# Kernel optimization log

Hardware: AMD Instinct MI355X
Metric: run time of the kernel (lower is better)

Reference implementation:

```python
import jax, jax.numpy as jnp
import numpy as np


def gru_layer(x, h0, Wih, Whh, bih, bhh):
    """Run a single-direction PyTorch-style GRU over x: [B,T,D] -> ([B,T,H], [B,H]).
    Gate order matches torch (r, z, n)."""
    xg = jnp.einsum('btd,gd->btg', x, Wih) + bih  # precompute input gates [B,T,3H]

    def step(h, gi):
        gh = h @ Whh.T + bhh
        ir, iz, inn = jnp.split(gi, 3, axis=-1)
        hr, hz, hn = jnp.split(gh, 3, axis=-1)
        r = jax.nn.sigmoid(ir + hr)
        z = jax.nn.sigmoid(iz + hz)
        n = jnp.tanh(inn + r * hn)
        h_new = (1.0 - z) * n + z * h
        return h_new, h_new

    hT, ys = jax.lax.scan(step, h0, jnp.swapaxes(xg, 0, 1))
    return jnp.swapaxes(ys, 0, 1), hT


def setup_inputs() -> dict:
    key = jax.random.key(0)
    ks = jax.random.split(key, 13)
    B, T, D, H = 64, 100, 75, 1024
    s = 0.02
    rn = lambda k, shp: (jax.random.normal(k, shp, jnp.float32) * s)
    return {
        'input_tensor': jax.random.normal(ks[0], (B, T, D), jnp.float32),
        'seq_len': jax.random.randint(ks[1], (B,), 1, T + 1, jnp.int32),
        'enc_Wih0': rn(ks[2], (2, 3 * H, D)),
        'enc_Whh0': rn(ks[3], (2, 3 * H, H)),
        'enc_b0': rn(ks[4], (2, 2, 3 * H)),
        'enc_Wih': rn(ks[5], (2, 2, 3 * H, 2 * H)),
        'enc_Whh': rn(ks[6], (2, 2, 3 * H, H)),
        'enc_b': rn(ks[7], (2, 2, 2, 3 * H)),
        'dec_Wih': rn(ks[8], (6 * H, D)),
        'dec_Whh': rn(ks[9], (6 * H, 2 * H)),
        'dec_b': rn(ks[10], (2, 6 * H)),
        'out_W': rn(ks[11], (D, 2 * H)),
        'out_b': rn(ks[12], (D,)),
    }


def reference(input_tensor, seq_len, enc_Wih0, enc_Whh0, enc_b0,
              enc_Wih, enc_Whh, enc_b, dec_Wih, dec_Whh, dec_b,
              out_W, out_b):
    B, T, D = input_tensor.shape
    H = enc_Whh0.shape[-1]
    h0 = jnp.zeros((B, H), input_tensor.dtype)

    # Encoder: the original feeds the bidirectional GRU one timestep at a time,
    # so BOTH direction parameter sets run left-to-right (degenerate bidir).
    yf, _ = gru_layer(input_tensor, h0, enc_Wih0[0], enc_Whh0[0], enc_b0[0, 0], enc_b0[0, 1])
    yb, _ = gru_layer(input_tensor, h0, enc_Wih0[1], enc_Whh0[1], enc_b0[1, 0], enc_b0[1, 1])
    y = jnp.concatenate([yf, yb], axis=-1)  # [B,T,2H]
    for l in range(enc_Wih.shape[0]):  # layers 1..num_layers-1
        yf, _ = gru_layer(y, h0, enc_Wih[l, 0], enc_Whh[l, 0], enc_b[l, 0, 0], enc_b[l, 0, 1])
        yb, _ = gru_layer(y, h0, enc_Wih[l, 1], enc_Whh[l, 1], enc_b[l, 1, 0], enc_b[l, 1, 1])
        y = jnp.concatenate([yf, yb], axis=-1)

    sl = jnp.clip(seq_len, 1, T)
    enc_hidden = y[jnp.arange(B), sl - 1][None]  # (1, B, 2H): last valid step per sample

    # Decoder: 1-layer GRU (hidden 2H) over a zeros input sequence, init = enc_hidden
    de_in = jnp.zeros_like(input_tensor)
    ys, _ = gru_layer(de_in, enc_hidden[0], dec_Wih, dec_Whh, dec_b[0], dec_b[1])
    dec_out = ys @ out_W.T + out_b  # [B,T,D]
    return (enc_hidden, dec_out)
```

## Files before the change

### kernel.cpp

```cpp
#include <hip/hip_runtime.h>
#include <math.h>

typedef unsigned short u16;
typedef unsigned long long u64;
typedef __attribute__((ext_vector_type(8))) short s16x8;
typedef __attribute__((ext_vector_type(4))) short s16x4;
typedef __attribute__((ext_vector_type(4))) float f4v;

__device__ __forceinline__ float bf2f(short u) {
    union { unsigned int i; float f; } v;
    v.i = ((unsigned int)(u16)u) << 16;
    return v.f;
}
__device__ __forceinline__ u16 f2bf(float f) {
    union { float f; unsigned int i; } v; v.f = f;
    unsigned int x = v.i;
    return (u16)((x + 0x7FFFu + ((x >> 16) & 1u)) >> 16);
}

__device__ __forceinline__ u64 coh_load_u64(const u16* p) {
    return __hip_atomic_load((const u64*)p, __ATOMIC_RELAXED, __HIP_MEMORY_SCOPE_AGENT);
}
__device__ __forceinline__ void coh_store_u64(u16* p, u64 v) {
    __hip_atomic_store((u64*)p, v, __ATOMIC_RELAXED, __HIP_MEMORY_SCOPE_AGENT);
}
__device__ __forceinline__ unsigned flag_load(const unsigned* p) {
    return __hip_atomic_load(p, __ATOMIC_RELAXED, __HIP_MEMORY_SCOPE_AGENT);
}
__device__ __forceinline__ void flag_store(unsigned* p, unsigned v) {
    __hip_atomic_store(p, v, __ATOMIC_RELAXED, __HIP_MEMORY_SCOPE_AGENT);
}

__device__ __forceinline__ void flag_barrier(unsigned* slot, int nblk, unsigned tgt) {
    __syncthreads();
    if (threadIdx.x == 0)
        flag_store(&slot[blockIdx.x], tgt);
    if (blockIdx.x == 0 && (int)threadIdx.x < 64) {
        int spins = 0;
        for (;;) {
            int ok = 1;
            for (int i = (int)threadIdx.x; i < nblk; i += 64)
                ok &= (flag_load(&slot[i]) >= tgt);
            if (__all(ok)) break;
            __builtin_amdgcn_s_sleep(2);
            if (++spins > (1 << 20)) break;
        }
        if (threadIdx.x == 0)
            flag_store(&slot[192], tgt);
    }
    if (threadIdx.x == 0) {
        int spins2 = 0;
        while (flag_load(&slot[192]) < tgt) {
            __builtin_amdgcn_s_sleep(1);
            if (++spins2 > (1 << 20)) break;
        }
    }
    __syncthreads();
    asm volatile("" ::: "memory");
}

__global__ void zero_bar(unsigned* p, int n) {
    int i = blockIdx.x * blockDim.x + threadIdx.x;
    if (i < n) p[i] = 0;
}

__global__ __launch_bounds__(256)
void cvt_bf16v(const float* __restrict__ src, u16* __restrict__ dst, int n4) {
    int i = blockIdx.x * 256 + threadIdx.x;
    int stride = gridDim.x * 256;
    for (; i < n4; i += stride) {
        f4v v = ((const f4v*)src)[i];
        s16x4 o;
#pragma unroll
        for (int j = 0; j < 4; ++j) o[j] = (short)f2bf(v[j]);
        ((s16x4*)dst)[i] = o;
    }
}

__global__ __launch_bounds__(256)
void cvt_pack(const float* __restrict__ src, u16* __restrict__ dst,
              int JT, int KB, int K)
{
    int fid = blockIdx.x * 4 + (threadIdx.x >> 6);
    int lane = threadIdx.x & 63;
    int nf = 3 * JT * KB;
    if (fid >= nf) return;
    int g = fid / (JT * KB);
    int rem = fid - g * JT * KB;
    int jt = rem / KB;
    int kb = rem - jt * KB;
    int j = jt * 16 + (lane & 15);
    int k = kb * 32 + (lane >> 4) * 8;
    const float* s = src + ((size_t)g * JT * 16 + j) * K + k;
    f4v a = *(const f4v*)s;
    f4v b = *(const f4v*)(s + 4);
    s16x8 o;
#pragma unroll
    for (int i = 0; i < 4; ++i) { o[i] = (short)f2bf(a[i]); o[4 + i] = (short)f2bf(b[i]); }
    *(s16x8*)(dst + (size_t)fid * 512 + lane * 8) = o;
}

__global__ __launch_bounds__(256)
void xg0_kernel(const float* __restrict__ x,
                const float* __restrict__ W,
                const float* __restrict__ bih,
                u16* __restrict__ xg)
{
    const int bt0 = blockIdx.x * 16;
    __shared__ float xl[16][76];
    for (int idx = threadIdx.x; idx < 16 * 75; idx += 256) {
        int r = idx / 75, k = idx % 75;
        xl[r][k] = x[(size_t)(bt0 + r) * 75 + k];
    }
    __syncthreads();
    for (int i = 0; i < 12; ++i) {
        int g = threadIdx.x + i * 256;
        const float* wr = W + (size_t)g * 75;
        float bv = bih[g];
        float acc[16];
#pragma unroll
        for (int r = 0; r < 16; ++r) acc[r] = bv;
        for (int k = 0; k < 75; ++k) {
            float w = wr[k];
#pragma unroll
            for (int r = 0; r < 16; ++r) acc[r] += xl[r][k] * w;
        }
#pragma unroll
        for (int r = 0; r < 16; ++r)
            xg[(size_t)(bt0 + r) * 3072 + g] = f2bf(acc[r]);
    }
}

__global__ __launch_bounds__(256)
void xg_gemm2(const u16* __restrict__ A, const float* __restrict__ Bm,
              const float* __restrict__ bias, u16* __restrict__ C, int K)
{
    __shared__ u16 Alds[128 * 40];
    __shared__ u16 Blds[64 * 40];
    const int bid = blockIdx.x;
    const int xcd = bid & 7;
    const int r = bid >> 3;
    const int n_t = xcd * 6 + r % 6;
    const int m_t = r / 6;
    const int m0 = m_t * 128;
    const int n0 = n_t * 64;
    const int tid = threadIdx.x;
    const int wv = tid >> 6;
    const int lane = tid & 63;
    const int kq = (lane >> 4) * 8;
    const int col = lane & 15;
    f4v acc[2][4];
#pragma unroll
    for (int am = 0; am < 2; ++am)
#pragma unroll
        for (int nt = 0; nt < 4; ++nt) acc[am][nt] = (f4v){0.f, 0.f, 0.f, 0.f};

    for (int k0 = 0; k0 < K; k0 += 32) {
#pragma unroll
        for (int i = 0; i < 2; ++i) {
            int c = tid * 2 + i;
            int row = c >> 2, kk = (c & 3) * 8;
            *(s16x8*)&Alds[row * 40 + kk] =
                *(const s16x8*)(A + (size_t)(m0 + row) * K + k0 + kk);
        }
        {
            int row = tid >> 2, kk = (tid & 3) * 8;
            f4v b0v = *(const f4v*)(Bm + (size_t)(n0 + row) * K + k0 + kk);
            f4v b1v = *(const f4v*)(Bm + (size_t)(n0 + row) * K + k0 + kk + 4);
            s16x8 bb;
#pragma unroll
            for (int i = 0; i < 4; ++i) { bb[i] = (short)f2bf(b0v[i]); bb[4 + i] = (short)f2bf(b1v[i]); }
            *(s16x8*)&Blds[row * 40 + kk] = bb;
        }
        __syncthreads();
        s16x8 a0 = *(const s16x8*)&Alds[(wv * 32 + (lane & 15)) * 40 + kq];
        s16x8 a1 = *(const s16x8*)&Alds[(wv * 32 + 16 + (lane & 15)) * 40 + kq];
#pragma unroll
        for (int nt = 0; nt < 4; ++nt) {
            s16x8 b = *(const s16x8*)&Blds[(nt * 16 + (lane & 15)) * 40 + kq];
            acc[0][nt] = __builtin_amdgcn_mfma_f32_16x16x32_bf16(a0, b, acc[0][nt], 0, 0, 0);
            acc[1][nt] = __builtin_amdgcn_mfma_f32_16x16x32_bf16(a1, b, acc[1][nt], 0, 0, 0);
        }
        __syncthreads();
    }
    const int rq = (lane >> 4) * 4;
#pragma unroll
    for (int am = 0; am < 2; ++am)
#pragma unroll
    for (int nt = 0; nt < 4; ++nt) {
        int n = n0 + nt * 16 + col;
        float bv = bias[n];
#pragma unroll
        for (int rg = 0; rg < 4; ++rg) {
            int m = m0 + wv * 32 + am * 16 + rq + rg;
            C[(size_t)m * 3072 + n] = f2bf(acc[am][nt][rg] + bv);
        }
    }
}

__global__ __launch_bounds__(256)
void enc_persist(const u16* __restrict__ Wp,
                 const float* __restrict__ bias,
                 const u16* __restrict__ xg,
                 u16* __restrict__ hbf,
                 u16* __restrict__ y,
                 int dir, unsigned* __restrict__ bar)
{
    __shared__ u16 Al[16 * 1024];
    __shared__ u16 OutE[16 * 64];
    const int tid = threadIdx.x;
    const int lane = tid & 63;
    const int wv = tid >> 6;
    const int xcd = blockIdx.x & 7;
    const int jg = xcd * 2 + ((blockIdx.x >> 3) & 1);
    const int bq = blockIdx.x >> 4;
    const int b0 = bq * 16;
    unsigned* flags = bar + bq * 64;
    const int jc = jg * 64 + wv * 16 + (lane & 15);
    const int jt = jg * 4 + wv;
    const int kq = (lane >> 4) * 8;
    const int arow = lane & 15;
    const int axor = (arow & 7) << 3;
    const float bhr = bias[3072 + jc];
    const float bhz = bias[4096 + jc];
    const float bhn = bias[5120 + jc];
    const u16* pW[3];
    pW[0] = Wp + ((size_t)(0 * 64 + jt) * 32) * 512 + lane * 8;
    pW[1] = Wp + ((size_t)(1 * 64 + jt) * 32) * 512 + lane * 8;
    pW[2] = Wp + ((size_t)(2 * 64 + jt) * 32) * 512 + lane * 8;
    const int brow = b0 + (lane >> 4) * 4;
    const int srow = tid >> 4;
    const int sci  = tid & 15;
    f4v hold = {0.f, 0.f, 0.f, 0.f};

    for (int t = 0; t < 100; ++t) {
        f4v aR = {0.f, 0.f, 0.f, 0.f}, aZ = aR, aN = aR;
        if (t > 0) {
            const u16* hb = hbf + (size_t)(t & 1) * 65536 + (size_t)b0 * 1024;
            {
                u64 v = coh_load_u64(hb + (size_t)srow * 1024 + jg * 64 + sci * 4);
                int c = srow * 128 + jg * 8 + (sci >> 1);
                int di = (c * 8) ^ ((srow & 7) << 3);
                *(u64*)&Al[di + (sci & 1) * 4] = v;
            }
            unsigned pending = 0xFFFFu & ~(1u << jg);
            int spins = 0;
            while (pending) {
                unsigned fv = flag_load(&flags[lane & 15]);
                unsigned ready = (unsigned)__ballot(fv >= (unsigned)t) & 0xFFFFu;
                unsigned newly = ready & pending;
                if (newly) {
                    u64 v[16];
#pragma unroll
                    for (int p = 0; p < 16; ++p)
                        if (newly & (1u << p))
                            v[p] = coh_load_u64(hb + (size_t)srow * 1024 + p * 64 + sci * 4);
#pragma unroll
                    for (int p = 0; p < 16; ++p)
                        if (newly & (1u << p)) {
                            int c = srow * 128 + p * 8 + (sci >> 1);
                            int di = (c * 8) ^ ((srow & 7) << 3);
                            *(u64*)&Al[di + (sci & 1) * 4] = v[p];
                        }
                    pending &= ~newly;
                }
                if (pending) {
                    __builtin_amdgcn_s_sleep(1);
                    if (++spins > (1 << 20)) break;
                }
            }
            __syncthreads();
            const int abase = arow * 1024 + kq;
            s16x8 W[2][3][4];
#pragma unroll
            for (int g = 0; g < 3; ++g)
#pragma unroll
                for (int q = 0; q < 4; ++q)
                    W[0][g][q] = *(const s16x8*)(pW[g] + (size_t)q * 512);
#pragma unroll
            for (int bt = 0; bt < 8; ++bt) {
                if (bt < 7) {
#pragma unroll
                    for (int g = 0; g < 3; ++g)
#pragma unroll
                        for (int q = 0; q < 4; ++q)
                            W[(bt + 1) & 1][g][q] =
                                *(const s16x8*)(pW[g] + (size_t)((bt + 1) * 4 + q) * 512);
                }
#pragma unroll
                for (int q = 0; q < 4; ++q) {
                    s16x8 av = *(const s16x8*)&Al[(abase + (bt * 4 + q) * 32) ^ axor];
                    aR = __builtin_amdgcn_mfma_f32_16x16x32_bf16(av, W[bt & 1][0][q], aR, 0, 0, 0);
                    aZ = __builtin_amdgcn_mfma_f32_16x16x32_bf16(av, W[bt & 1][1][q], aZ, 0, 0, 0);
                    aN = __builtin_amdgcn_mfma_f32_16x16x32_bf16(av, W[bt & 1][2][q], aN, 0, 0, 0);
                }
            }
        }
#pragma unroll
        for (int r = 0; r < 4; ++r) {
            int b = brow + r;
            const u16* xr = xg + ((size_t)b * 100 + t) * 3072;
            float pr = bf2f((short)xr[jc]) + aR[r] + bhr;
            float pz = bf2f((short)xr[1024 + jc]) + aZ[r] + bhz;
            float pn = bf2f((short)xr[2048 + jc]);
            float rg = 1.f / (1.f + expf(-pr));
            float zg = 1.f / (1.f + expf(-pz));
            float ng = tanhf(pn + rg * (aN[r] + bhn));
            float hnew = (1.f - zg) * ng + zg * hold[r];
            hold[r] = hnew;
            OutE[((lane >> 4) * 4 + r) * 64 + wv * 16 + (lane & 15)] = f2bf(hnew);
        }
        __syncthreads();
        if (tid < 128) {
            int bl = tid >> 3, jl = (tid & 7) * 8;
            s16x8 v = *(const s16x8*)&OutE[bl * 64 + jl];
            const u64* pv = (const u64*)&v;
            u16* hw = hbf + (size_t)((t + 1) & 1) * 65536
                    + (size_t)(b0 + bl) * 1024 + jg * 64 + jl;
            coh_store_u64(hw, pv[0]);
            coh_store_u64(hw + 4, pv[1]);
            *(s16x8*)(y + ((size_t)(b0 + bl) * 100 + t) * 2048
                        + (size_t)dir * 1024 + jg * 64 + jl) = v;
        }
        if (t < 99) {
            __syncthreads();
            if (tid == 0) flag_store(&flags[jg], (unsigned)(t + 1));
        }
    }
}

__global__ __launch_bounds__(256)
void dec_persist(const u16* __restrict__ Wp,
                 const float* __restrict__ db,
                 const float* __restrict__ h32,
                 u16* __restrict__ hbf,
                 u16* __restrict__ ys,
                 unsigned* __restrict__ bar)
{
    __shared__ u16 Al[16 * 2048];
    __shared__ u16 OutD[16 * 64];
    const int tid = threadIdx.x;
    const int lane = tid & 63;
    const int wv = tid >> 6;
    const int xcd = blockIdx.x & 7;
    const int idx = blockIdx.x >> 3;
    const int jg = xcd * 4 + (idx & 3);
    const int b0 = (idx >> 2) * 16;
    const int jc = jg * 64 + wv * 16 + (lane & 15);
    const int jt = jg * 4 + wv;
    const int kq = (lane >> 4) * 8;
    const int arow = lane & 15;
    const int axor = (arow & 7) << 3;
    const float gir = db[jc]        + db[6144 + jc];
    const float giz = db[2048 + jc] + db[8192 + jc];
    const float gin = db[4096 + jc];
    const float bhn = db[10240 + jc];
    const u16* pR = Wp + ((size_t)(0 * 128 + jt) * 64) * 512 + lane * 8;
    const u16* pZ = Wp + ((size_t)(1 * 128 + jt) * 64) * 512 + lane * 8;
    const u16* pN = Wp + ((size_t)(2 * 128 + jt) * 64) * 512 + lane * 8;
    f4v hold;
#pragma unroll
    for (int r = 0; r < 4; ++r)
        hold[r] = h32[(size_t)(b0 + (lane >> 4) * 4 + r) * 2048 + jc];

    for (int t = 0; t < 100; ++t) {
        const u16* hb = hbf + (size_t)(t & 1) * 131072 + (size_t)b0 * 2048;
#pragma unroll
        for (int h = 0; h < 2; ++h) {
            u64 tmp[16];
#pragma unroll
            for (int g = 0; g < 8; ++g) {
                int c = tid + (h * 8 + g) * 256;
                const u16* gp = hb + (size_t)(c >> 8) * 2048 + (c & 255) * 8;
                tmp[2 * g]     = coh_load_u64(gp);
                tmp[2 * g + 1] = coh_load_u64(gp + 4);
            }
#pragma unroll
            for (int g = 0; g < 8; ++g) {
                int c = tid + (h * 8 + g) * 256;
                int di = (c * 8) ^ (((c >> 8) & 7) << 3);
                *(u64*)&Al[di]     = tmp[2 * g];
                *(u64*)&Al[di + 4] = tmp[2 * g + 1];
            }
        }
        __syncthreads();
        f4v aR = {0.f, 0.f, 0.f, 0.f}, aZ = aR, aN = aR;
        const int abase = arow * 2048 + kq;
        s16x8 cR = *(const s16x8*)(pR);
        s16x8 cZ = *(const s16x8*)(pZ);
        s16x8 cN = *(const s16x8*)(pN);
        for (int kb = 0; kb < 64; ++kb) {
            int kn = (kb + 1 < 64) ? kb + 1 : kb;
            s16x8 nR = *(const s16x8*)(pR + (size_t)kn * 512);
            s16x8 nZ = *(const s16x8*)(pZ + (size_t)kn * 512);
            s16x8 nN = *(const s16x8*)(pN + (size_t)kn * 512);
            s16x8 av = *(const s16x8*)&Al[(abase + kb * 32) ^ axor];
            aR = __builtin_amdgcn_mfma_f32_16x16x32_bf16(av, cR, aR, 0, 0, 0);
            aZ = __builtin_amdgcn_mfma_f32_16x16x32_bf16(av, cZ, aZ, 0, 0, 0);
            aN = __builtin_amdgcn_mfma_f32_16x16x32_bf16(av, cN, aN, 0, 0, 0);
            cR = nR; cZ = nZ; cN = nN;
        }
        __syncthreads();
#pragma unroll
        for (int r = 0; r < 4; ++r) {
            float pr = gir + aR[r];
            float pz = giz + aZ[r];
            float rg = 1.f / (1.f + expf(-pr));
            float zg = 1.f / (1.f + expf(-pz));
            float ng = tanhf(gin + rg * (aN[r] + bhn));
            float hnew = (1.f - zg) * ng + zg * hold[r];
            hold[r] = hnew;
            OutD[((lane >> 4) * 4 + r) * 64 + wv * 16 + (lane & 15)] = f2bf(hnew);
        }
        __syncthreads();
        if (tid < 128) {
            int bl = tid >> 3, jl = (tid & 7) * 8;
            s16x8 v = *(const s16x8*)&OutD[bl * 64 + jl];
            const u64* pv = (const u64*)&v;
            u16* hw = hbf + (size_t)((t + 1) & 1) * 131072
                    + (size_t)(b0 + bl) * 2048 + jg * 64 + jl;
            coh_store_u64(hw, pv[0]);
            coh_store_u64(hw + 4, pv[1]);
            *(s16x8*)(ys + ((size_t)(b0 + bl) * 100 + t) * 2048 + jg * 64 + jl) = v;
        }
        if (t < 99) flag_barrier(bar, 128, (unsigned)(t + 1));
    }
}

__global__ __launch_bounds__(256)
void gather_kernel(const int* __restrict__ seq_len, const u16* __restrict__ y,
                   float* __restrict__ out_enc, float* __restrict__ h32d,
                   u16* __restrict__ hbfd)
{
    int idx = blockIdx.x * 256 + threadIdx.x;
    int b = idx >> 11, j = idx & 2047;
    int s = seq_len[b];
    s = s < 1 ? 1 : (s > 100 ? 100 : s);
    u16 v = y[((size_t)b * 100 + (s - 1)) * 2048 + j];
    float f = bf2f((short)v);
    out_enc[idx] = f;
    h32d[idx] = f;
    hbfd[idx] = v;
}

__global__ __launch_bounds__(256)
void proj_kernel(const u16* __restrict__ ys, const float* __restrict__ oW,
                 const float* __restrict__ oB, float* __restrict__ dec_out)
{
    const int r0 = blockIdx.x * 8;
    __shared__ float yl[8][2048];
    __shared__ float psum[3][8][76];
    for (int idx = threadIdx.x; idx < 2048; idx += 256) {
        int rr = idx >> 8, cc = idx & 255;
        s16x8 v = ((const s16x8*)(ys + (size_t)(r0 + rr) * 2048))[cc];
#pragma unroll
        for (int i = 0; i < 8; ++i) yl[rr][cc * 8 + i] = bf2f(v[i]);
    }
    __syncthreads();
    if (threadIdx.x < 225) {
        int d = threadIdx.x % 75, seg = threadIdx.x / 75;
        int ks = seg * 683, ke = ks + 683 < 2048 ? ks + 683 : 2048;
        const float* wr = oW + (size_t)d * 2048;
        float acc[8] = {0.f, 0.f, 0.f, 0.f, 0.f, 0.f, 0.f, 0.f};
        for (int k = ks; k < ke; ++k) {
            float w = wr[k];
#pragma unroll
            for (int r = 0; r < 8; ++r) acc[r] += yl[r][k] * w;
        }
#pragma unroll
        for (int r = 0; r < 8; ++r) psum[seg][r][d] = acc[r];
    }
    __syncthreads();
    for (int idx = threadIdx.x; idx < 600; idx += 256) {
        int r = idx / 75, d = idx % 75;
        dec_out[(size_t)(r0 + r) * 75 + d] =
            psum[0][r][d] + psum[1][r][d] + psum[2][r][d] + oB[d];
    }
}

__device__ __forceinline__ void gemv3_f32(const float* __restrict__ w0,
                                          const float* __restrict__ w1,
                                          const float* __restrict__ w2,
                                          const f4v* __restrict__ hv,
                                          int n4, float& a0, float& a1, float& a2)
{
    for (int k = 0; k < n4; ++k) {
        f4v h4 = hv[k];
        f4v x0 = *(const f4v*)(w0 + k * 4);
        f4v x1 = *(const f4v*)(w1 + k * 4);
        f4v x2 = *(const f4v*)(w2 + k * 4);
        a0 += h4[0]*x0[0] + h4[1]*x0[1] + h4[2]*x0[2] + h4[3]*x0[3];
        a1 += h4[0]*x1[0] + h4[1]*x1[1] + h4[2]*x1[2] + h4[3]*x1[3];
        a2 += h4[0]*x2[0] + h4[1]*x2[1] + h4[2]*x2[2] + h4[3]*x2[3];
    }
}
__device__ __forceinline__ float dot_w32_v32(const float* __restrict__ w,
                                             const float* __restrict__ v, int n)
{
    float a = 0.f;
    for (int k = 0; k < n; ++k) a += w[k] * v[k];
    return a;
}
__device__ __forceinline__ float dot_w32_vbf(const float* __restrict__ w,
                                             const u16* __restrict__ v, int n8)
{
    float a = 0.f;
    for (int k8 = 0; k8 < n8; ++k8) {
        s16x8 v8 = *(const s16x8*)(v + k8 * 8);
        f4v w0 = *(const f4v*)(w + k8 * 8);
        f4v w1 = *(const f4v*)(w + k8 * 8 + 4);
        a += w0[0]*bf2f(v8[0]) + w0[1]*bf2f(v8[1]) + w0[2]*bf2f(v8[2]) + w0[3]*bf2f(v8[3])
           + w1[0]*bf2f(v8[4]) + w1[1]*bf2f(v8[5]) + w1[2]*bf2f(v8[6]) + w1[3]*bf2f(v8[7]);
    }
    return a;
}

__global__ __launch_bounds__(512)
void enc_scan_fused(int t,
                    const float* __restrict__ h_in, float* __restrict__ h_out,
                    const float* __restrict__ Whh, size_t whh_stride,
                    const float* __restrict__ Wih, size_t wih_stride, int Kin,
                    const float* __restrict__ xf, const u16* __restrict__ xb,
                    const float* __restrict__ bias, int bias_stride,
                    u16* __restrict__ y)
{
    const int dir = blockIdx.z;
    const int jt = blockIdx.x;
    const int b0 = blockIdx.y * 16;
    __shared__ float hlds[16][1024];
    const float* hin = h_in + (size_t)dir * 65536 + (size_t)b0 * 1024;
    if (t == 0) {
        f4v z = {0.f, 0.f, 0.f, 0.f};
        for (int idx = threadIdx.x; idx < 4096; idx += 512) ((f4v*)hlds)[idx] = z;
    } else {
        for (int idx = threadIdx.x; idx < 4096; idx += 512)
            ((f4v*)hlds)[idx] = ((const f4v*)hin)[idx];
    }
    __syncthreads();
    const int jl = threadIdx.x & 31;
    const int j  = jt * 32 + jl;
    const int bp = threadIdx.x >> 5;
    const float* wd = Whh + (size_t)dir * whh_stride;
    float a0 = 0.f, a1 = 0.f, a2 = 0.f;
    gemv3_f32(wd + (size_t)j * 1024, wd + (size_t)(1024 + j) * 1024,
              wd + (size_t)(2048 + j) * 1024, (const f4v*)&hlds[bp][0], 256, a0, a1, a2);
    const float* bd = bias + dir * bias_stride;
    const float* wi = Wih + (size_t)dir * wih_stride;
    const int gb = b0 + bp;
    float gi[3];
#pragma unroll
    for (int g = 0; g < 3; ++g) {
        const float* wr = wi + (size_t)(g * 1024 + j) * Kin;
        float s;
        if (xf) s = dot_w32_v32(wr, xf + ((size_t)gb * 100 + t) * Kin, Kin);
        else    s = dot_w32_vbf(wr, xb + ((size_t)gb * 100 + t) * Kin, Kin >> 3);
        gi[g] = bd[g * 1024 + j] + s;
    }
    const float* bhh = bd + 3072;
    float pr = gi[0] + a0 + bhh[j];
    float pz = gi[1] + a1 + bhh[1024 + j];
    float rg = 1.f / (1.f + expf(-pr));
    float zg = 1.f / (1.f + expf(-pz));
    float ng = tanhf(gi[2] + rg * (a2 + bhh[2048 + j]));
    float hold = hlds[bp][j];
    float hnew = (1.f - zg) * ng + zg * hold;
    h_out[(size_t)dir * 65536 + (size_t)gb * 1024 + j] = hnew;
    y[((size_t)gb * 100 + t) * 2048 + (size_t)dir * 1024 + j] = f2bf(hnew);
}

__global__ __launch_bounds__(512)
void dec_scan_step(int t, const float* __restrict__ h_in, float* __restrict__ h_out,
                   const float* __restrict__ Whh, const float* __restrict__ db,
                   u16* __restrict__ ys)
{
    const int jt = blockIdx.x;
    const int b0 = blockIdx.y * 16;
    __shared__ float hlds[16][1024];
    const int jl = threadIdx.x & 31;
    const int j  = jt * 32 + jl;
    const int bp = threadIdx.x >> 5;
    float a0 = 0.f, a1 = 0.f, a2 = 0.f;
    float hold = 0.f;
    for (int kc = 0; kc < 2; ++kc) {
        for (int idx = threadIdx.x; idx < 4096; idx += 512) {
            int rr = idx >> 8, cc = idx & 255;
            ((f4v*)hlds)[idx] = *(const f4v*)(h_in + (size_t)(b0 + rr) * 2048 + kc * 1024 + cc * 4);
        }
        __syncthreads();
        if ((j >> 10) == kc) hold = hlds[bp][j & 1023];
        const float* wb = Whh + kc * 1024;
        gemv3_f32(wb + (size_t)j * 2048, wb + (size_t)(2048 + j) * 2048,
                  wb + (size_t)(4096 + j) * 2048, (const f4v*)&hlds[bp][0], 256, a0, a1, a2);
        __syncthreads();
    }
    const int gb = b0 + bp;
    float pr = db[j] + a0 + db[6144 + j];
    float pz = db[2048 + j] + a1 + db[6144 + 2048 + j];
    float rg = 1.f / (1.f + expf(-pr));
    float zg = 1.f / (1.f + expf(-pz));
    float ng = tanhf(db[4096 + j] + rg * (a2 + db[6144 + 4096 + j]));
    float hnew = (1.f - zg) * ng + zg * hold;
    h_out[(size_t)gb * 2048 + j] = hnew;
    ys[((size_t)gb * 100 + t) * 2048 + j] = f2bf(hnew);
}

extern "C" void kernel_launch(void* const* d_in, const int* in_sizes, int n_in,
                              void* d_out, int out_size, void* d_ws, size_t ws_size,
                              hipStream_t stream)
{
    const float* x    = (const float*)d_in[0];
    const int*   sl   = (const int*)d_in[1];
    const float* Wih0 = (const float*)d_in[2];
    const float* Whh0 = (const float*)d_in[3];
    const float* b0   = (const float*)d_in[4];
    const float* Wih  = (const float*)d_in[5];
    const float* Whh  = (const float*)d_in[6];
    const float* bE   = (const float*)d_in[7];
    const float* dWhh = (const float*)d_in[9];
    const float* dB   = (const float*)d_in[10];
    const float* oW   = (const float*)d_in[11];
    const float* oB   = (const float*)d_in[12];
    float* out_enc = (float*)d_out;
    float* dec_out = (float*)d_out + 131072;

    char* ws = (char*)d_ws;
    const size_t XG_OFF   = 0;
    const size_t YA_OFF   = 39321600;
    const size_t YB_OFF   = 65536000;
    const size_t WC_OFF   = 91750400;
    const size_t HBFE_OFF = 98566144;
    const size_t H32D_OFF = 98828288;
    const size_t HBFD_OFF = 99876864;
    const size_t BAR_OFF  = 100401152;
    const size_t NEED     = 100408320;

    dim3 blk256(256), blk512(512);

    if (ws_size >= NEED) {
        u16*   xg   = (u16*)(ws + XG_OFF);
        u16*   y_a  = (u16*)(ws + YA_OFF);
        u16*   y_b  = (u16*)(ws + YB_OFF);
        u16*   Wc   = (u16*)(ws + WC_OFF);
        u16*   hbfE = (u16*)(ws + HBFE_OFF);
        float* h32D = (float*)(ws + H32D_OFF);
        u16*   hbfD = (u16*)(ws + HBFD_OFF);
        unsigned* bar = (unsigned*)(ws + BAR_OFF);

        zero_bar<<<dim3(7), blk256, 0, stream>>>(bar, 1792);

        int slot = 0;
        for (int l = 0; l < 3; ++l) {
            const u16* y_in = (l == 0) ? (const u16*)0 : ((l == 1) ? y_a : y_b);
            u16* y_out      = (l == 2) ? y_a : ((l == 0) ? y_a : y_b);
            for (int d = 0; d < 2; ++d) {
                const float* Wsrc = (l == 0) ? (Whh0 + (size_t)d * 3145728)
                                             : (Whh + ((size_t)(l - 1) * 2 + d) * 3145728);
                const float* bias = (l == 0) ? (b0 + (size_t)d * 6144)
                                             : (bE + (size_t)(l - 1) * 12288 + (size_t)d * 6144);
                cvt_pack<<<dim3(1536), blk256, 0, stream>>>(Wsrc, Wc, 64, 32, 1024);
                if (l == 0)
                    xg0_kernel<<<dim3(400), blk256, 0, stream>>>(
                        x, Wih0 + (size_t)d * 230400, b0 + (size_t)d * 6144, xg);
                else
                    xg_gemm2<<<dim3(2400), blk256, 0, stream>>>(
                        y_in, Wih + ((size_t)(l - 1) * 2 + d) * 6291456, bias, xg, 2048);
                enc_persist<<<dim3(64), blk256, 0, stream>>>(
                    Wc, bias, xg, hbfE, y_out, d, bar + (size_t)slot * 256);
                ++slot;
            }
        }
        gather_kernel<<<dim3(512), blk256, 0, stream>>>(sl, y_a, out_enc, h32D, hbfD);
        u16* decW = (u16*)(ws + XG_OFF);
        cvt_pack<<<dim3(6144), blk256, 0, stream>>>(dWhh, decW, 128, 64, 2048);
        dec_persist<<<dim3(128), blk256, 0, stream>>>(decW, dB, h32D, hbfD, y_b,
                                                      bar + (size_t)6 * 256);
        proj_kernel<<<dim3(800), blk256, 0, stream>>>(y_b, oW, oB, dec_out);
    } else {
        const size_t Y_B = 26214400;
        u16*   y_a  = (u16*)ws;
        u16*   y_b  = (u16*)(ws + Y_B);
        float* hE   = (float*)(ws + 2 * Y_B);
        float* h32D = (float*)(ws + 2 * Y_B + 1048576);
        u16*   hbfD = (u16*)(ws + 2 * Y_B + 2097152);

        for (int t = 0; t < 100; ++t) {
            int pp = t & 1;
            enc_scan_fused<<<dim3(32, 4, 2), blk512, 0, stream>>>(
                t, hE + (size_t)pp * 131072, hE + (size_t)(pp ^ 1) * 131072,
                Whh0, (size_t)3145728, Wih0, (size_t)230400, 75, x, (const u16*)0,
                b0, 6144, y_a);
        }
        for (int l = 0; l < 2; ++l) {
            const u16* yin = (l == 0) ? y_a : y_b;
            u16* yout      = (l == 0) ? y_b : y_a;
            for (int t = 0; t < 100; ++t) {
                int pp = t & 1;
                enc_scan_fused<<<dim3(32, 4, 2), blk512, 0, stream>>>(
                    t, hE + (size_t)pp * 131072, hE + (size_t)(pp ^ 1) * 131072,
                    Whh + (size_t)l * 2 * 3145728, (size_t)3145728,
                    Wih + (size_t)l * 2 * 6291456, (size_t)6291456, 2048,
                    (const float*)0, yin, bE + (size_t)l * 12288, 6144, yout);
            }
        }
        gather_kernel<<<dim3(512), blk256, 0, stream>>>(sl, y_a, out_enc, h32D, hbfD);
        for (int t = 0; t < 100; ++t) {
            int pp = t & 1;
            dec_scan_step<<<dim3(64, 4), blk512, 0, stream>>>(
                t, h32D + (size_t)pp * 131072, h32D + (size_t)(pp ^ 1) * 131072, dWhh, dB, y_b);
        }
        proj_kernel<<<dim3(800), blk256, 0, stream>>>(y_b, oW, oB, dec_out);
    }
}
```

Baseline: 7.885 ms.

## Fuse input-gate GEMM into persistent encoder and run both directions concurrently

Removes the separate xg precompute kernels and computes the input-gate projection inside the persistent recurrent kernel each timestep, reading layer inputs straight from the previous layer's output. Both directions of a layer now run in one 128-block launch instead of two sequential 64-block launches, which halves the number of serialized recurrences. The cost is extra per-step work on the critical path: a 2048-deep GEMM per step streaming Wih from global memory, plus more LDS use (a 64KB Yl buffer). The Whh inner loop is also changed from register double-buffered tiles to simple one-ahead prefetching.

```diff
diff --git a/kernel.cpp b/kernel.cpp
--- a/kernel.cpp
+++ b/kernel.cpp
@@ -65,21 +65,8 @@
 }
 
 __global__ __launch_bounds__(256)
-void cvt_bf16v(const float* __restrict__ src, u16* __restrict__ dst, int n4) {
-    int i = blockIdx.x * 256 + threadIdx.x;
-    int stride = gridDim.x * 256;
-    for (; i < n4; i += stride) {
-        f4v v = ((const f4v*)src)[i];
-        s16x4 o;
-#pragma unroll
-        for (int j = 0; j < 4; ++j) o[j] = (short)f2bf(v[j]);
-        ((s16x4*)dst)[i] = o;
-    }
-}
-
-__global__ __launch_bounds__(256)
 void cvt_pack(const float* __restrict__ src, u16* __restrict__ dst,
-              int JT, int KB, int K)
+              int JT, int KB, int Kstride, int Ksrc)
 {
     int fid = blockIdx.x * 4 + (threadIdx.x >> 6);
     int lane = threadIdx.x & 63;
@@ -91,159 +78,110 @@
     int kb = rem - jt * KB;
     int j = jt * 16 + (lane & 15);
     int k = kb * 32 + (lane >> 4) * 8;
-    const float* s = src + ((size_t)g * JT * 16 + j) * K + k;
-    f4v a = *(const f4v*)s;
-    f4v b = *(const f4v*)(s + 4);
+    const float* s = src + ((size_t)g * JT * 16 + j) * Kstride + k;
     s16x8 o;
-#pragma unroll
-    for (int i = 0; i < 4; ++i) { o[i] = (short)f2bf(a[i]); o[4 + i] = (short)f2bf(b[i]); }
+    if (k + 8 <= Ksrc) {
+        f4v a = *(const f4v*)s;
+        f4v b = *(const f4v*)(s + 4);
+#pragma unroll
+        for (int i = 0; i < 4; ++i) { o[i] = (short)f2bf(a[i]); o[4 + i] = (short)f2bf(b[i]); }
+    } else {
+#pragma unroll
+        for (int e = 0; e < 8; ++e)
+            o[e] = (k + e < Ksrc) ? (short)f2bf(s[e]) : (short)0;
+    }
     *(s16x8*)(dst + (size_t)fid * 512 + lane * 8) = o;
 }
 
 __global__ __launch_bounds__(256)
-void xg0_kernel(const float* __restrict__ x,
-                const float* __restrict__ W,
-                const float* __restrict__ bih,
-                u16* __restrict__ xg)
-{
-    const int bt0 = blockIdx.x * 16;
-    __shared__ float xl[16][76];
-    for (int idx = threadIdx.x; idx < 16 * 75; idx += 256) {
-        int r = idx / 75, k = idx % 75;
-        xl[r][k] = x[(size_t)(bt0 + r) * 75 + k];
-    }
-    __syncthreads();
-    for (int i = 0; i < 12; ++i) {
-        int g = threadIdx.x + i * 256;
-        const float* wr = W + (size_t)g * 75;
-        float bv = bih[g];
-        float acc[16];
-#pragma unroll
-        for (int r = 0; r < 16; ++r) acc[r] = bv;
-        for (int k = 0; k < 75; ++k) {
-            float w = wr[k];
-#pragma unroll
-            for (int r = 0; r < 16; ++r) acc[r] += xl[r][k] * w;
-        }
-#pragma unroll
-        for (int r = 0; r < 16; ++r)
-            xg[(size_t)(bt0 + r) * 3072 + g] = f2bf(acc[r]);
-    }
-}
-
-__global__ __launch_bounds__(256)
-void xg_gemm2(const u16* __restrict__ A, const float* __restrict__ Bm,
-              const float* __restrict__ bias, u16* __restrict__ C, int K)
-{
-    __shared__ u16 Alds[128 * 40];
-    __shared__ u16 Blds[64 * 40];
-    const int bid = blockIdx.x;
-    const int xcd = bid & 7;
-    const int r = bid >> 3;
-    const int n_t = xcd * 6 + r % 6;
-    const int m_t = r / 6;
-    const int m0 = m_t * 128;
-    const int n0 = n_t * 64;
-    const int tid = threadIdx.x;
-    const int wv = tid >> 6;
-    const int lane = tid & 63;
-    const int kq = (lane >> 4) * 8;
-    const int col = lane & 15;
-    f4v acc[2][4];
-#pragma unroll
-    for (int am = 0; am < 2; ++am)
-#pragma unroll
-        for (int nt = 0; nt < 4; ++nt) acc[am][nt] = (f4v){0.f, 0.f, 0.f, 0.f};
-
-    for (int k0 = 0; k0 < K; k0 += 32) {
-#pragma unroll
-        for (int i = 0; i < 2; ++i) {
-            int c = tid * 2 + i;
-            int row = c >> 2, kk = (c & 3) * 8;
-            *(s16x8*)&Alds[row * 40 + kk] =
-                *(const s16x8*)(A + (size_t)(m0 + row) * K + k0 + kk);
-        }
-        {
-            int row = tid >> 2, kk = (tid & 3) * 8;
-            f4v b0v = *(const f4v*)(Bm + (size_t)(n0 + row) * K + k0 + kk);
-            f4v b1v = *(const f4v*)(Bm + (size_t)(n0 + row) * K + k0 + kk + 4);
-            s16x8 bb;
-#pragma unroll
-            for (int i = 0; i < 4; ++i) { bb[i] = (short)f2bf(b0v[i]); bb[4 + i] = (short)f2bf(b1v[i]); }
-            *(s16x8*)&Blds[row * 40 + kk] = bb;
-        }
-        __syncthreads();
-        s16x8 a0 = *(const s16x8*)&Alds[(wv * 32 + (lane & 15)) * 40 + kq];
-        s16x8 a1 = *(const s16x8*)&Alds[(wv * 32 + 16 + (lane & 15)) * 40 + kq];
-#pragma unroll
-        for (int nt = 0; nt < 4; ++nt) {
-            s16x8 b = *(const s16x8*)&Blds[(nt * 16 + (lane & 15)) * 40 + kq];
-            acc[0][nt] = __builtin_amdgcn_mfma_f32_16x16x32_bf16(a0, b, acc[0][nt], 0, 0, 0);
-            acc[1][nt] = __builtin_amdgcn_mfma_f32_16x16x32_bf16(a1, b, acc[1][nt], 0, 0, 0);
-        }
-        __syncthreads();
-    }
-    const int rq = (lane >> 4) * 4;
-#pragma unroll
-    for (int am = 0; am < 2; ++am)
-#pragma unroll
-    for (int nt = 0; nt < 4; ++nt) {
-        int n = n0 + nt * 16 + col;
-        float bv = bias[n];
-#pragma unroll
-        for (int rg = 0; rg < 4; ++rg) {
-            int m = m0 + wv * 32 + am * 16 + rq + rg;
-            C[(size_t)m * 3072 + n] = f2bf(acc[am][nt][rg] + bv);
-        }
-    }
-}
-
-__global__ __launch_bounds__(256)
-void enc_persist(const u16* __restrict__ Wp,
-                 const float* __restrict__ bias,
-                 const u16* __restrict__ xg,
-                 u16* __restrict__ hbf,
-                 u16* __restrict__ y,
-                 int dir, unsigned* __restrict__ bar)
-{
+void enc_fused(const u16* __restrict__ WihP, int wih_dfrags,
+               const u16* __restrict__ WhhP,
+               const float* __restrict__ bias,
+               const float* __restrict__ x,
+               const u16* __restrict__ yin,
+               u16* __restrict__ hbf,
+               u16* __restrict__ yout,
+               unsigned* __restrict__ bar)
+{
+    __shared__ u16 Yl[16 * 2048];
     __shared__ u16 Al[16 * 1024];
     __shared__ u16 OutE[16 * 64];
     const int tid = threadIdx.x;
     const int lane = tid & 63;
     const int wv = tid >> 6;
     const int xcd = blockIdx.x & 7;
-    const int jg = xcd * 2 + ((blockIdx.x >> 3) & 1);
-    const int bq = blockIdx.x >> 4;
+    const int dir = xcd >> 2;
+    const int idx = blockIdx.x >> 3;
+    const int jgd = (xcd & 3) * 4 + (idx & 3);
+    const int bq = idx >> 2;
     const int b0 = bq * 16;
-    unsigned* flags = bar + bq * 64;
-    const int jc = jg * 64 + wv * 16 + (lane & 15);
-    const int jt = jg * 4 + wv;
+    unsigned* flags = bar + (dir * 4 + bq) * 64;
+    const int jc = jgd * 64 + wv * 16 + (lane & 15);
+    const int jt = jgd * 4 + wv;
     const int kq = (lane >> 4) * 8;
     const int arow = lane & 15;
     const int axor = (arow & 7) << 3;
-    const float bhr = bias[3072 + jc];
-    const float bhz = bias[4096 + jc];
-    const float bhn = bias[5120 + jc];
+    const float* bd = bias + dir * 6144;
+    const float biasR = bd[jc] + bd[3072 + jc];
+    const float biasZ = bd[1024 + jc] + bd[4096 + jc];
+    const float bihN = bd[2048 + jc];
+    const float bhhN = bd[5120 + jc];
+    const u16* WihD = WihP + (size_t)dir * wih_dfrags * 512;
+    const u16* WhhD = WhhP + (size_t)dir * (3 * 64 * 32) * 512;
+    const int kbin = wih_dfrags / 192;
+    const u16* pXW[3];
     const u16* pW[3];
-    pW[0] = Wp + ((size_t)(0 * 64 + jt) * 32) * 512 + lane * 8;
-    pW[1] = Wp + ((size_t)(1 * 64 + jt) * 32) * 512 + lane * 8;
-    pW[2] = Wp + ((size_t)(2 * 64 + jt) * 32) * 512 + lane * 8;
+#pragma unroll
+    for (int g = 0; g < 3; ++g) {
+        pXW[g] = WihD + ((size_t)(g * 64 + jt) * kbin) * 512 + lane * 8;
+        pW[g]  = WhhD + ((size_t)(g * 64 + jt) * 32) * 512 + lane * 8;
+    }
     const int brow = b0 + (lane >> 4) * 4;
     const int srow = tid >> 4;
     const int sci  = tid & 15;
+    u16* hbfD = hbf + (size_t)dir * 131072;
     f4v hold = {0.f, 0.f, 0.f, 0.f};
 
+    if (x) {
+        for (int i = tid; i < 16 * 21; i += 256) {
+            int r = i / 21, k = 75 + i % 21;
+            Yl[r * 96 + k] = 0;
+        }
+    }
+
     for (int t = 0; t < 100; ++t) {
-        f4v aR = {0.f, 0.f, 0.f, 0.f}, aZ = aR, aN = aR;
+        if (x) {
+            for (int i = tid; i < 1200; i += 256) {
+                int r = i / 75, k = i % 75;
+                Yl[r * 96 + k] = f2bf(x[((size_t)(b0 + r) * 100 + t) * 75 + k]);
+            }
+        } else {
+#pragma unroll
+            for (int h2 = 0; h2 < 2; ++h2) {
+                s16x8 tmp[8];
+#pragma unroll
+                for (int g2 = 0; g2 < 8; ++g2) {
+                    int c = tid + (h2 * 8 + g2) * 256;
+                    int row = c >> 8, coli = c & 255;
+                    tmp[g2] = *(const s16x8*)(yin + ((size_t)(b0 + row) * 100 + t) * 2048 + coli * 8);
+                }
+#pragma unroll
+                for (int g2 = 0; g2 < 8; ++g2) {
+                    int c = tid + (h2 * 8 + g2) * 256;
+                    int di = (c * 8) ^ (((c >> 8) & 7) << 3);
+                    *(s16x8*)&Yl[di] = tmp[g2];
+                }
+            }
+        }
         if (t > 0) {
-            const u16* hb = hbf + (size_t)(t & 1) * 65536 + (size_t)b0 * 1024;
+            const u16* hb = hbfD + (size_t)(t & 1) * 65536 + (size_t)b0 * 1024;
             {
-                u64 v = coh_load_u64(hb + (size_t)srow * 1024 + jg * 64 + sci * 4);
-                int c = srow * 128 + jg * 8 + (sci >> 1);
+                u64 v = coh_load_u64(hb + (size_t)srow * 1024 + jgd * 64 + sci * 4);
+                int c = srow * 128 + jgd * 8 + (sci >> 1);
                 int di = (c * 8) ^ ((srow & 7) << 3);
                 *(u64*)&Al[di + (sci & 1) * 4] = v;
             }
-            unsigned pending = 0xFFFFu & ~(1u << jg);
+            unsigned pending = 0xFFFFu & ~(1u << jgd);
             int spins = 0;
             while (pending) {
                 unsigned fv = flag_load(&flags[lane & 15]);
@@ -269,43 +207,63 @@
                     if (++spins > (1 << 20)) break;
                 }
             }
-            __syncthreads();
-            const int abase = arow * 1024 + kq;
-            s16x8 W[2][3][4];
-#pragma unroll
-            for (int g = 0; g < 3; ++g)
-#pragma unroll
-                for (int q = 0; q < 4; ++q)
-                    W[0][g][q] = *(const s16x8*)(pW[g] + (size_t)q * 512);
-#pragma unroll
-            for (int bt = 0; bt < 8; ++bt) {
-                if (bt < 7) {
-#pragma unroll
-                    for (int g = 0; g < 3; ++g)
-#pragma unroll
-                        for (int q = 0; q < 4; ++q)
-                            W[(bt + 1) & 1][g][q] =
-                                *(const s16x8*)(pW[g] + (size_t)((bt + 1) * 4 + q) * 512);
-                }
-#pragma unroll
-                for (int q = 0; q < 4; ++q) {
-                    s16x8 av = *(const s16x8*)&Al[(abase + (bt * 4 + q) * 32) ^ axor];
-                    aR = __builtin_amdgcn_mfma_f32_16x16x32_bf16(av, W[bt & 1][0][q], aR, 0, 0, 0);
-                    aZ = __builtin_amdgcn_mfma_f32_16x16x32_bf16(av, W[bt & 1][1][q], aZ, 0, 0, 0);
-                    aN = __builtin_amdgcn_mfma_f32_16x16x32_bf16(av, W[bt & 1][2][q], aN, 0, 0, 0);
-                }
+        }
+        __syncthreads();
+        f4v xR = {0.f, 0.f, 0.f, 0.f}, xZ = xR, xN = xR;
+        if (x) {
+            const int abase = arow * 96 + kq;
+#pragma unroll
+            for (int kb = 0; kb < 3; ++kb) {
+                s16x8 av = *(const s16x8*)&Yl[abase + kb * 32];
+                s16x8 wR = *(const s16x8*)(pXW[0] + (size_t)kb * 512);
+                s16x8 wZ = *(const s16x8*)(pXW[1] + (size_t)kb * 512);
+                s16x8 wN = *(const s16x8*)(pXW[2] + (size_t)kb * 512);
+                xR = __builtin_amdgcn_mfma_f32_16x16x32_bf16(av, wR, xR, 0, 0, 0);
+                xZ = __builtin_amdgcn_mfma_f32_16x16x32_bf16(av, wZ, xZ, 0, 0, 0);
+                xN = __builtin_amdgcn_mfma_f32_16x16x32_bf16(av, wN, xN, 0, 0, 0);
+            }
+        } else {
+            const int abase = arow * 2048 + kq;
+            s16x8 cR = *(const s16x8*)(pXW[0]);
+            s16x8 cZ = *(const s16x8*)(pXW[1]);
+            s16x8 cN = *(const s16x8*)(pXW[2]);
+            for (int kb = 0; kb < 64; ++kb) {
+                int kn = (kb + 1 < 64) ? kb + 1 : kb;
+                s16x8 nR = *(const s16x8*)(pXW[0] + (size_t)kn * 512);
+                s16x8 nZ = *(const s16x8*)(pXW[1] + (size_t)kn * 512);
+                s16x8 nN = *(const s16x8*)(pXW[2] + (size_t)kn * 512);
+                s16x8 av = *(const s16x8*)&Yl[(abase + kb * 32) ^ axor];
+                xR = __builtin_amdgcn_mfma_f32_16x16x32_bf16(av, cR, xR, 0, 0, 0);
+                xZ = __builtin_amdgcn_mfma_f32_16x16x32_bf16(av, cZ, xZ, 0, 0, 0);
+                xN = __builtin_amdgcn_mfma_f32_16x16x32_bf16(av, cN, xN, 0, 0, 0);
+                cR = nR; cZ = nZ; cN = nN;
+            }
+        }
+        f4v aR = {0.f, 0.f, 0.f, 0.f}, aZ = aR, aN = aR;
+        if (t > 0) {
+            const int abase2 = arow * 1024 + kq;
+            s16x8 cR = *(const s16x8*)(pW[0]);
+            s16x8 cZ = *(const s16x8*)(pW[1]);
+            s16x8 cN = *(const s16x8*)(pW[2]);
+            for (int kb = 0; kb < 32; ++kb) {
+                int kn = (kb + 1 < 32) ? kb + 1 : kb;
+                s16x8 nR = *(const s16x8*)(pW[0] + (size_t)kn * 512);
+                s16x8 nZ = *(const s16x8*)(pW[1] + (size_t)kn * 512);
+                s16x8 nN = *(const s16x8*)(pW[2] + (size_t)kn * 512);
+                s16x8 av = *(const s16x8*)&Al[(abase2 + kb * 32) ^ axor];
+                aR = __builtin_amdgcn_mfma_f32_16x16x32_bf16(av, cR, aR, 0, 0, 0);
+                aZ = __builtin_amdgcn_mfma_f32_16x16x32_bf16(av, cZ, aZ, 0, 0, 0);
+                aN = __builtin_amdgcn_mfma_f32_16x16x32_bf16(av, cN, aN, 0, 0, 0);
+                cR = nR; cZ = nZ; cN = nN;
             }
         }
 #pragma unroll
         for (int r = 0; r < 4; ++r) {
-            int b = brow + r;
-            const u16* xr = xg + ((size_t)b * 100 + t) * 3072;
-            float pr = bf2f((short)xr[jc]) + aR[r] + bhr;
-            float pz = bf2f((short)xr[1024 + jc]) + aZ[r] + bhz;
-            float pn = bf2f((short)xr[2048 + jc]);
+            float pr = xR[r] + aR[r] + biasR;
+            float pz = xZ[r] + aZ[r] + biasZ;
             float rg = 1.f / (1.f + expf(-pr));
             float zg = 1.f / (1.f + expf(-pz));
-            float ng = tanhf(pn + rg * (aN[r] + bhn));
+            float ng = tanhf(xN[r] + bihN + rg * (aN[r] + bhhN));
             float hnew = (1.f - zg) * ng + zg * hold[r];
             hold[r] = hnew;
             OutE[((lane >> 4) * 4 + r) * 64 + wv * 16 + (lane & 15)] = f2bf(hnew);
@@ -315,17 +273,18 @@
             int bl = tid >> 3, jl = (tid & 7) * 8;
             s16x8 v = *(const s16x8*)&OutE[bl * 64 + jl];
             const u64* pv = (const u64*)&v;
-            u16* hw = hbf + (size_t)((t + 1) & 1) * 65536
-                    + (size_t)(b0 + bl) * 1024 + jg * 64 + jl;
+            u16* hw = hbfD + (size_t)((t + 1) & 1) * 65536
+                    + (size_t)(b0 + bl) * 1024 + jgd * 64 + jl;
             coh_store_u64(hw, pv[0]);
             coh_store_u64(hw + 4, pv[1]);
-            *(s16x8*)(y + ((size_t)(b0 + bl) * 100 + t) * 2048
-                        + (size_t)dir * 1024 + jg * 64 + jl) = v;
+            *(s16x8*)(yout + ((size_t)(b0 + bl) * 100 + t) * 2048
+                          + (size_t)dir * 1024 + jgd * 64 + jl) = v;
         }
         if (t < 99) {
             __syncthreads();
-            if (tid == 0) flag_store(&flags[jg], (unsigned)(t + 1));
-        }
+            if (tid == 0) flag_store(&flags[jgd], (unsigned)(t + 1));
+        }
+        (void)brow;
     }
 }
 
@@ -624,56 +583,58 @@
     float* dec_out = (float*)d_out + 131072;
 
     char* ws = (char*)d_ws;
-    const size_t XG_OFF   = 0;
-    const size_t YA_OFF   = 39321600;
-    const size_t YB_OFF   = 65536000;
-    const size_t WC_OFF   = 91750400;
-    const size_t HBFE_OFF = 98566144;
-    const size_t H32D_OFF = 98828288;
-    const size_t HBFD_OFF = 99876864;
-    const size_t BAR_OFF  = 100401152;
-    const size_t NEED     = 100408320;
+    const size_t YA_OFF   = 0;
+    const size_t YB_OFF   = 26214400;
+    const size_t WIH_OFF  = 52428800;
+    const size_t WHH_OFF  = 77594624;
+    const size_t HBE_OFF  = 90177536;
+    const size_t H32D_OFF = 90701824;
+    const size_t HBFD_OFF = 91750400;
+    const size_t BAR_OFF  = 92274688;
+    const size_t NEED     = 92281856;
 
     dim3 blk256(256), blk512(512);
 
     if (ws_size >= NEED) {
-        u16*   xg   = (u16*)(ws + XG_OFF);
         u16*   y_a  = (u16*)(ws + YA_OFF);
         u16*   y_b  = (u16*)(ws + YB_OFF);
-        u16*   Wc   = (u16*)(ws + WC_OFF);
-        u16*   hbfE = (u16*)(ws + HBFE_OFF);
+        u16*   WihB = (u16*)(ws + WIH_OFF);
+        u16*   WhhB = (u16*)(ws + WHH_OFF);
+        u16*   hbfE = (u16*)(ws + HBE_OFF);
         float* h32D = (float*)(ws + H32D_OFF);
         u16*   hbfD = (u16*)(ws + HBFD_OFF);
         unsigned* bar = (unsigned*)(ws + BAR_OFF);
 
         zero_bar<<<dim3(7), blk256, 0, stream>>>(bar, 1792);
 
-        int slot = 0;
         for (int l = 0; l < 3; ++l) {
-            const u16* y_in = (l == 0) ? (const u16*)0 : ((l == 1) ? y_a : y_b);
-            u16* y_out      = (l == 2) ? y_a : ((l == 0) ? y_a : y_b);
             for (int d = 0; d < 2; ++d) {
-                const float* Wsrc = (l == 0) ? (Whh0 + (size_t)d * 3145728)
-                                             : (Whh + ((size_t)(l - 1) * 2 + d) * 3145728);
-                const float* bias = (l == 0) ? (b0 + (size_t)d * 6144)
-                                             : (bE + (size_t)(l - 1) * 12288 + (size_t)d * 6144);
-                cvt_pack<<<dim3(1536), blk256, 0, stream>>>(Wsrc, Wc, 64, 32, 1024);
+                const float* WhhSrc = (l == 0) ? (Whh0 + (size_t)d * 3145728)
+                                               : (Whh + ((size_t)(l - 1) * 2 + d) * 3145728);
+                cvt_pack<<<dim3(1536), blk256, 0, stream>>>(
+                    WhhSrc, WhhB + (size_t)d * 3145728, 64, 32, 1024, 1024);
                 if (l == 0)
-                    xg0_kernel<<<dim3(400), blk256, 0, stream>>>(
-                        x, Wih0 + (size_t)d * 230400, b0 + (size_t)d * 6144, xg);
+                    cvt_pack<<<dim3(144), blk256, 0, stream>>>(
+                        Wih0 + (size_t)d * 230400, WihB + (size_t)d * 294912, 64, 3, 75, 75);
                 else
-                    xg_gemm2<<<dim3(2400), blk256, 0, stream>>>(
-                        y_in, Wih + ((size_t)(l - 1) * 2 + d) * 6291456, bias, xg, 2048);
-                enc_persist<<<dim3(64), blk256, 0, stream>>>(
-                    Wc, bias, xg, hbfE, y_out, d, bar + (size_t)slot * 256);
-                ++slot;
-            }
+                    cvt_pack<<<dim3(3072), blk256, 0, stream>>>(
+                        Wih + ((size_t)(l - 1) * 2 + d) * 6291456,
+                        WihB + (size_t)d * 6291456, 64, 64, 2048, 2048);
+            }
+            const float* bias = (l == 0) ? b0 : (bE + (size_t)(l - 1) * 12288);
+            const u16* yin = (l == 0) ? (const u16*)0 : ((l == 1) ? y_a : y_b);
+            u16* yout      = (l == 2) ? y_a : ((l == 0) ? y_a : y_b);
+            int wih_dfrags = (l == 0) ? 576 : 12288;
+            enc_fused<<<dim3(128), blk256, 0, stream>>>(
+                WihB, wih_dfrags, WhhB, bias,
+                (l == 0) ? x : (const float*)0, yin,
+                hbfE, yout, bar + (size_t)l * 512);
         }
         gather_kernel<<<dim3(512), blk256, 0, stream>>>(sl, y_a, out_enc, h32D, hbfD);
-        u16* decW = (u16*)(ws + XG_OFF);
-        cvt_pack<<<dim3(6144), blk256, 0, stream>>>(dWhh, decW, 128, 64, 2048);
+        u16* decW = WihB;
+        cvt_pack<<<dim3(6144), blk256, 0, stream>>>(dWhh, decW, 128, 64, 2048, 2048);
         dec_persist<<<dim3(128), blk256, 0, stream>>>(decW, dB, h32D, hbfD, y_b,
-                                                      bar + (size_t)6 * 256);
+                                                      bar + (size_t)1536);
         proj_kernel<<<dim3(800), blk256, 0, stream>>>(y_b, oW, oB, dec_out);
     } else {
         const size_t Y_B = 26214400;
```

After: 8.624 ms. 9.4% more time.
